# Kernel optimization log

Hardware: AMD Instinct MI355X
Metric: run time of the kernel (lower is better)

## Reference

```python
import jax, jax.numpy as jnp
import numpy as np

ALPHA = 0.2
NEG_INF = -9e15


def setup_inputs() -> dict:
    key = jax.random.key(0)
    k1, k2, k3, k4 = jax.random.split(key, 4)
    B, N, C_IN, C_OUT, R, H = 8, 1024, 256, 256, 4, 4
    node_feats = jax.random.normal(k1, (B, N, C_IN), dtype=jnp.float32)
    adj_matrix = jax.random.randint(k2, (B, N, N, R), 0, 2, dtype=jnp.int32)
    # xavier_uniform with gain=1.414 for Linear(c_in, c_out) weights
    lim_w = 1.414 * np.sqrt(6.0 / (C_IN + C_OUT))
    W = jax.random.uniform(k3, (R, C_IN, C_OUT), minval=-lim_w, maxval=lim_w, dtype=jnp.float32)
    c_per = C_OUT // H
    lim_a = 1.414 * np.sqrt(6.0 / (H + 2 * c_per))
    a = jax.random.uniform(k4, (R, H, 2 * c_per), minval=-lim_a, maxval=lim_a, dtype=jnp.float32)
    return {"node_feats": node_feats, "adj_matrix": adj_matrix, "W": W, "a": a}


def reference(node_feats, adj_matrix, W, a):
    B, N, _ = node_feats.shape
    R, H = a.shape[0], a.shape[1]
    C = a.shape[2] // 2  # per-head feature dim
    out = jnp.zeros((B, N, H, C), dtype=node_feats.dtype)
    for r in range(R):
        # per-relation projection: [B,N,H,C]
        f = jnp.einsum('bnc,cd->bnd', node_feats, W[r]).reshape(B, N, H, C)
        a_l, a_r = a[r, :, :C], a[r, :, C:]
        # attention logit decomposes: a . [f_i || f_j] = a_l . f_i + a_r . f_j
        li = jnp.einsum('bnhc,hc->bnh', f, a_l)  # source-node term
        lj = jnp.einsum('bnhc,hc->bnh', f, a_r)  # target-node term
        logits = jax.nn.leaky_relu(li[:, :, None, :] + lj[:, None, :, :], ALPHA)  # [B,N,N,H]
        mask = adj_matrix[..., r] != 0  # [B,N,N]
        logits = jnp.where(mask[..., None], logits, NEG_INF)
        probs = jax.nn.softmax(logits, axis=2)
        out = out + jnp.einsum('bijh,bjhc->bihc', probs, f)
    # concat_heads=True
    return out.reshape(B, N, H * C)
```

## Files before the change

### kernel.cpp

```cpp
#include <hip/hip_runtime.h>
#include <math.h>

#define Bsz 8
#define Nn 1024
#define CIN 256
#define COUT 256
#define NR 4
#define NH 4

typedef unsigned short u16;
typedef __attribute__((ext_vector_type(8))) short bf16x8;
typedef __attribute__((ext_vector_type(4))) float f32x4;
typedef __attribute__((ext_vector_type(2))) float f32x2;

#define OFF_LIP (16u << 20)
#define OFF_LJP ((16u << 20) + (512u << 10))
#define OFF_ADJM (17u << 20)
#define OFF_XBF (21u << 20)
#define OFF_WBFT (25u << 20)
#define OFF_WAL ((25u << 20) + (512u << 10))
#define OFF_WAR ((25u << 20) + (528u << 10))
#define OFF_OUTR (26u << 20)

#define LOG2E 1.4426950408889634f

__device__ __forceinline__ short f2bf(float x) {
  union { float f; unsigned u; } v; v.f = x;
  unsigned r = (v.u + 0x7FFFu + ((v.u >> 16) & 1u)) >> 16;
  return (short)r;
}

__device__ __forceinline__ float fast_exp2(float x) {
#if __has_builtin(__builtin_amdgcn_exp2f)
  return __builtin_amdgcn_exp2f(x);
#else
  return exp2f(x);
#endif
}

__device__ __forceinline__ int sbfe1(unsigned v, int bit) {
#if __has_builtin(__builtin_amdgcn_sbfe)
  return __builtin_amdgcn_sbfe((int)v, bit, 1);
#else
  return ((int)(v << (31 - bit))) >> 31;
#endif
}

__device__ __forceinline__ unsigned perm_hi16(unsigned hi, unsigned lo) {
#if __has_builtin(__builtin_amdgcn_perm)
  return __builtin_amdgcn_perm(hi, lo, 0x07060302u);
#else
  return (lo >> 16) | (hi & 0xFFFF0000u);
#endif
}

__device__ __forceinline__ void gl_lds16(const void* g, void* l) {
  __builtin_amdgcn_global_load_lds(
      (const __attribute__((address_space(1))) unsigned int*)(unsigned long long)g,
      (__attribute__((address_space(3))) unsigned int*)(unsigned int)(unsigned long long)l,
      16, 0, 0);
}

__global__ __launch_bounds__(256, 8)
void gatt_pack(const int4* __restrict__ adj4, unsigned long long* __restrict__ adjm) {
  const int t = threadIdx.x;
  const int wid = blockIdx.x * 4 + (t >> 6);
  const int lane = t & 63;
  const int jw = wid & 15;
  const int i = (wid >> 4) & 1023;
  const int b = wid >> 14;
  const int j = jw * 64 + lane;
  const int4 av = adj4[(size_t)(b * Nn + i) * Nn + j];
  const unsigned long long b0 = __ballot(av.x != 0);
  const unsigned long long b1 = __ballot(av.y != 0);
  const unsigned long long b2 = __ballot(av.z != 0);
  const unsigned long long b3 = __ballot(av.w != 0);
  if (lane < 4) {
    unsigned long long v = (lane == 0) ? b0 : (lane == 1) ? b1 : (lane == 2) ? b2 : b3;
    adjm[((size_t)((b * Nn + i) * NR + lane)) * 16 + jw] = v;
  }
}

__global__ __launch_bounds__(256, 4)
void gatt_prep(const float* __restrict__ W, const float* __restrict__ a,
               u16* __restrict__ WbfT, float* __restrict__ wa_l,
               float* __restrict__ wa_r) {
  const int t = threadIdx.x;
  if (blockIdx.x < 32) {
    const int r = blockIdx.x >> 3, kc = blockIdx.x & 7;
    u16 pk[32];
#pragma unroll 8
    for (int kk = 0; kk < 32; ++kk)
      pk[kk] = (u16)f2bf(W[(size_t)r * 65536 + (size_t)(kc * 32 + kk) * COUT + t]);
    u16* dst = WbfT + (size_t)r * 65536 + (size_t)t * CIN + kc * 32;
#pragma unroll
    for (int q = 0; q < 4; ++q) *(int4*)(dst + q * 8) = *(int4*)(pk + q * 8);
  } else {
    const int cb = blockIdx.x - 32;
    const int r = cb >> 2, h = cb & 3;
    float sl = 0.f, sr = 0.f;
    const float* Wp = W + (size_t)r * 65536 + (size_t)t * COUT + h * 64;
    const float* ap = a + r * 512 + h * 128;
#pragma unroll 8
    for (int c = 0; c < 64; ++c) {
      const float wv = Wp[c];
      sl = fmaf(wv, ap[c], sl);
      sr = fmaf(wv, ap[64 + c], sr);
    }
    wa_l[(size_t)cb * CIN + t] = sl;
    wa_r[(size_t)cb * CIN + t] = sr;
  }
}

__global__ __launch_bounds__(256, 4)
void gatt_logitx(const float* __restrict__ X, const float4* __restrict__ wal4,
                 const float4* __restrict__ war4, float* __restrict__ Lip,
                 float* __restrict__ Ljp, u16* __restrict__ Xbf) {
  __shared__ float Xs[16 * 260];
  const int t = threadIdx.x;
  const int row0 = blockIdx.x * 16;
  {
    const int il = t >> 4, kq = t & 15;
    const float4* xp = (const float4*)(X + (size_t)(row0 + il) * CIN + kq * 16);
    float4 v[4];
    u16 pk[16];
#pragma unroll
    for (int u = 0; u < 4; ++u) {
      v[u] = xp[u];
      pk[u * 4 + 0] = (u16)f2bf(v[u].x);
      pk[u * 4 + 1] = (u16)f2bf(v[u].y);
      pk[u * 4 + 2] = (u16)f2bf(v[u].z);
      pk[u * 4 + 3] = (u16)f2bf(v[u].w);
    }
    float4* dst = (float4*)(Xs + il * 260 + kq * 16);
#pragma unroll
    for (int u = 0; u < 4; ++u) dst[u] = v[u];
    u16* xb = Xbf + (size_t)(row0 + il) * CIN + kq * 16;
    *(int4*)xb = *(int4*)pk;
    *(int4*)(xb + 8) = *(int4*)(pk + 8);
  }
  __syncthreads();
  const int rl = t >> 4, combo = t & 15;
  float li = 0.f, lj = 0.f;
#pragma unroll 8
  for (int k4 = 0; k4 < 64; ++k4) {
    const float4 x4 = *(const float4*)(Xs + rl * 260 + k4 * 4);
    const float4 wl = wal4[combo * 64 + k4];
    const float4 wr = war4[combo * 64 + k4];
    li += x4.x * wl.x + x4.y * wl.y + x4.z * wl.z + x4.w * wl.w;
    lj += x4.x * wr.x + x4.y * wr.y + x4.z * wr.z + x4.w * wr.w;
  }
  const int g = row0 + rl, b = g >> 10, n = g & 1023;
  const size_t idx = ((size_t)(combo * Bsz + b)) * Nn + n;
  Lip[idx] = li * LOG2E;
  Ljp[idx] = lj * LOG2E;
}

__global__ __launch_bounds__(256)
void gatt_fgemm(const u16* __restrict__ Xbf, const u16* __restrict__ WbfT,
                u16* __restrict__ fTf) {
  __shared__ u16 lds_w[8192];
  __shared__ u16 lds_x[2048];
  const int t = threadIdx.x;
  const int r = blockIdx.x & 3, b = (blockIdx.x >> 2) & 7, ntl = blockIdx.x >> 5;
  const int n0 = ntl * 64;
  const int g0 = b * Nn + n0;
  const int lane = t & 63, w = t >> 6;
  const int m = lane & 15, quad = lane >> 4;
  const int cw = w * 64;
  const int xq = quad ^ (m & 3);

  const u16* Wsrc = WbfT + (size_t)r * 65536;
  f32x4 acc[4][4];
#pragma unroll
  for (int ct = 0; ct < 4; ++ct)
#pragma unroll
    for (int nt = 0; nt < 4; ++nt) acc[ct][nt] = (f32x4){0.f, 0.f, 0.f, 0.f};

  for (int kc = 0; kc < 8; ++kc) {
    __syncthreads();
#pragma unroll
    for (int q = 0; q < 4; ++q) {
      const int s = q * 256 + t;
      const int c = s >> 2, ks = (s & 3) ^ (c & 3);
      gl_lds16(Wsrc + (size_t)c * CIN + kc * 32 + ks * 8, lds_w + s * 8);
    }
    {
      const int s = t;
      const int n = s >> 2, ks = (s & 3) ^ (n & 3);
      gl_lds16(Xbf + (size_t)(g0 + n) * CIN + kc * 32 + ks * 8, lds_x + s * 8);
    }
    __syncthreads();

    bf16x8 af[4], bfr[4];
#pragma unroll
    for (int ct = 0; ct < 4; ++ct)
      af[ct] = *(const bf16x8*)(lds_w + (cw + ct * 16 + m) * 32 + xq * 8);
#pragma unroll
    for (int nt = 0; nt < 4; ++nt)
      bfr[nt] = *(const bf16x8*)(lds_x + (nt * 16 + m) * 32 + xq * 8);
#pragma unroll
    for (int ct = 0; ct < 4; ++ct)
#pragma unroll
      for (int nt = 0; nt < 4; ++nt)
        acc[ct][nt] = __builtin_amdgcn_mfma_f32_16x16x32_bf16(af[ct], bfr[nt], acc[ct][nt], 0, 0, 0);
  }

  u16* fragbase = fTf + (size_t)(((r * Bsz + b) * 4 + w) * 128) * 512;
#pragma unroll
  for (int ct = 0; ct < 4; ++ct) {
#pragma unroll
    for (int ntf = 0; ntf < 4; ++ntf) {
      const int j = n0 + ntf * 16 + m;
      const int jb = j >> 5;
      const int qt = ((ntf & 1) << 1) | (m >> 3);
      const int e = m & 7;
      u16* dst = fragbase + (size_t)((jb * 4 + ct) * 512) + (qt * 16 + quad * 4) * 8 + e;
#pragma unroll
      for (int p = 0; p < 4; ++p) dst[p * 8] = (u16)f2bf(acc[ct][ntf][p]);
    }
  }
}

__global__ __launch_bounds__(256, 4)
void gatt_attn(const unsigned long long* __restrict__ adjm,
               const u16* __restrict__ fTf, const float* __restrict__ Lip,
               const float* __restrict__ Ljp, float* __restrict__ outr) {
  __shared__ float ljs[4 * 1024];

  const int t = threadIdx.x;
  const int comb = blockIdx.x & 31;
  const int b = comb >> 2, r = comb & 3;
  const int i0 = (blockIdx.x >> 5) * 32;
  const int h = t >> 6, lane = t & 63;
  const int m = lane & 15, quad = lane >> 4;
  const int qo = quad * 8;

  {
#pragma unroll
    for (int q = 0; q < 4; ++q) {
      const int s = q * 256 + t;
      const int hh = s >> 8, off = s & 255;
      ((float4*)ljs)[hh * 256 + off] =
          ((const float4*)(Ljp + ((size_t)((r * NH + hh) * Bsz + b)) * Nn))[off];
    }
  }
  __syncthreads();

  const float* lipb = Lip + ((size_t)((r * NH + h) * Bsz + b)) * Nn;
  const float li0 = lipb[i0 + m];
  const float li1 = lipb[i0 + 16 + m];
  const unsigned long long* amp0 = adjm + ((size_t)((b * Nn + i0 + m) * NR + r)) * 16;
  const unsigned long long* amp1 = adjm + ((size_t)((b * Nn + i0 + 16 + m) * NR + r)) * 16;
  const bf16x8* fp = (const bf16x8*)fTf + (size_t)(((r * Bsz + b) * 4 + h)) * 8192;
  const float* ljh = ljs + h * Nn;

  bf16x8 ones;
#pragma unroll
  for (int e = 0; e < 8; ++e) ones[e] = (short)0x3F80;

  f32x4 acc[2][4], den[2];
#pragma unroll
  for (int iw = 0; iw < 2; ++iw) {
    den[iw] = (f32x4){0.f, 0.f, 0.f, 0.f};
#pragma unroll
    for (int nt = 0; nt < 4; ++nt) acc[iw][nt] = (f32x4){0.f, 0.f, 0.f, 0.f};
  }

  for (int jq = 0; jq < 16; ++jq) {
    const uint2 mw0 = *(const uint2*)(amp0 + jq);
    const uint2 mw1 = *(const uint2*)(amp1 + jq);
#pragma unroll
    for (int half = 0; half < 2; ++half) {
      const int jb = jq * 2 + half;
      const unsigned w0 = half ? mw0.y : mw0.x;
      const unsigned w1 = half ? mw1.y : mw1.x;
      const f32x2* lj2p = (const f32x2*)(ljh + jb * 32 + qo);
      bf16x8 bfr[4];
#pragma unroll
      for (int nt = 0; nt < 4; ++nt) bfr[nt] = fp[(jb * 4 + nt) * 64 + lane];
#pragma unroll
      for (int iw = 0; iw < 2; ++iw) {
        const float liv = iw ? li1 : li0;
        const unsigned mb = (iw ? w1 : w0) >> qo;
        const f32x2 li2 = {liv, liv};
        unsigned afu[4];
#pragma unroll
        for (int pr = 0; pr < 4; ++pr) {
          const f32x2 s2 = li2 + lj2p[pr];
          const f32x2 s02 = s2 * 0.2f;
          const float t0 = fmaxf(s2.x, s02.x);
          const float t1 = fmaxf(s2.y, s02.y);
          const unsigned e0 =
              __float_as_uint(fast_exp2(t0)) & (unsigned)sbfe1(mb, 2 * pr);
          const unsigned e1 =
              __float_as_uint(fast_exp2(t1)) & (unsigned)sbfe1(mb, 2 * pr + 1);
          afu[pr] = perm_hi16(e1, e0);
        }
        union { unsigned u[4]; bf16x8 v; } af;
        af.u[0] = afu[0]; af.u[1] = afu[1]; af.u[2] = afu[2]; af.u[3] = afu[3];
        den[iw] = __builtin_amdgcn_mfma_f32_16x16x32_bf16(af.v, ones, den[iw], 0, 0, 0);
#pragma unroll
        for (int nt = 0; nt < 4; ++nt)
          acc[iw][nt] = __builtin_amdgcn_mfma_f32_16x16x32_bf16(af.v, bfr[nt], acc[iw][nt], 0, 0, 0);
      }
    }
  }

#pragma unroll
  for (int iw = 0; iw < 2; ++iw) {
#pragma unroll
    for (int p = 0; p < 4; ++p) {
      const float inv = __builtin_amdgcn_rcpf(den[iw][p]);
      const int i = i0 + iw * 16 + quad * 4 + p;
      float* op = outr + (((size_t)(r * Bsz + b) * Nn) + i) * COUT + h * 64 + m;
#pragma unroll
      for (int nt = 0; nt < 4; ++nt) op[nt * 16] = acc[iw][nt][p] * inv;
    }
  }
}

__global__ __launch_bounds__(256, 8)
void gatt_reduce(const float4* __restrict__ outr4, float4* __restrict__ out4) {
  const int idx = blockIdx.x * 256 + threadIdx.x;
  float4 v0 = outr4[idx];
  float4 v1 = outr4[idx + 524288];
  float4 v2 = outr4[idx + 2 * 524288];
  float4 v3 = outr4[idx + 3 * 524288];
  out4[idx] = make_float4(v0.x + v1.x + v2.x + v3.x, v0.y + v1.y + v2.y + v3.y,
                          v0.z + v1.z + v2.z + v3.z, v0.w + v1.w + v2.w + v3.w);
}

extern "C" void kernel_launch(void* const* d_in, const int* in_sizes, int n_in,
                              void* d_out, int out_size, void* d_ws, size_t ws_size,
                              hipStream_t stream) {
  const float* X = (const float*)d_in[0];
  const int4* adj4 = (const int4*)d_in[1];
  const float* W = (const float*)d_in[2];
  const float* a = (const float*)d_in[3];
  float* out = (float*)d_out;

  char* ws = (char*)d_ws;
  u16* fTf = (u16*)ws;
  float* Lip = (float*)(ws + OFF_LIP);
  float* Ljp = (float*)(ws + OFF_LJP);
  unsigned long long* adjm = (unsigned long long*)(ws + OFF_ADJM);
  u16* Xbf = (u16*)(ws + OFF_XBF);
  u16* WbfT = (u16*)(ws + OFF_WBFT);
  float* wa_l = (float*)(ws + OFF_WAL);
  float* wa_r = (float*)(ws + OFF_WAR);
  float* outr = (float*)(ws + OFF_OUTR);

  gatt_pack<<<dim3(32768), dim3(256), 0, stream>>>(adj4, adjm);
  gatt_prep<<<dim3(48), dim3(256), 0, stream>>>(W, a, WbfT, wa_l, wa_r);
  gatt_logitx<<<dim3(512), dim3(256), 0, stream>>>(X, (const float4*)wa_l,
                                                   (const float4*)wa_r, Lip, Ljp, Xbf);
  gatt_fgemm<<<dim3(512), dim3(256), 0, stream>>>(Xbf, WbfT, fTf);
  gatt_attn<<<dim3(1024), dim3(256), 0, stream>>>(adjm, fTf, Lip, Ljp, outr);
  gatt_reduce<<<dim3(2048), dim3(256), 0, stream>>>((const float4*)outr, (float4*)out);
}
```

Measured before the change: 294.7 us.

## Fuse relation loop into attention, drop reduce kernel, merge pack/prep, LDS-free fgemm

The attention kernel now loops over all four relations per block and accumulates the normalized outputs in registers. This removes the per-relation partial-output buffer and the separate reduction kernel. The pack and weight-prep kernels are merged into one launch. W is pre-laid out in MFMA fragment order so the projection GEMM loads operands directly from global memory without LDS staging. Each attention block now covers 16 rows instead of 32 and no longer caches Lj in LDS, so it issues fewer blocks with less per-block reuse of f fragments.

```diff
diff --git a/kernel.cpp b/kernel.cpp
--- a/kernel.cpp
+++ b/kernel.cpp
@@ -17,10 +17,9 @@
 #define OFF_LJP ((16u << 20) + (512u << 10))
 #define OFF_ADJM (17u << 20)
 #define OFF_XBF (21u << 20)
-#define OFF_WBFT (25u << 20)
+#define OFF_WFRAG (25u << 20)
 #define OFF_WAL ((25u << 20) + (512u << 10))
 #define OFF_WAR ((25u << 20) + (528u << 10))
-#define OFF_OUTR (26u << 20)
 
 #define LOG2E 1.4426950408889634f
 
@@ -54,49 +53,46 @@
 #endif
 }
 
-__device__ __forceinline__ void gl_lds16(const void* g, void* l) {
-  __builtin_amdgcn_global_load_lds(
-      (const __attribute__((address_space(1))) unsigned int*)(unsigned long long)g,
-      (__attribute__((address_space(3))) unsigned int*)(unsigned int)(unsigned long long)l,
-      16, 0, 0);
-}
-
-__global__ __launch_bounds__(256, 8)
-void gatt_pack(const int4* __restrict__ adj4, unsigned long long* __restrict__ adjm) {
+__global__ __launch_bounds__(256, 4)
+void gatt_packprep(const int4* __restrict__ adj4, const float* __restrict__ W,
+                   const float* __restrict__ a, unsigned long long* __restrict__ adjm,
+                   u16* __restrict__ Wfrag, float* __restrict__ wa_l,
+                   float* __restrict__ wa_r) {
   const int t = threadIdx.x;
-  const int wid = blockIdx.x * 4 + (t >> 6);
-  const int lane = t & 63;
-  const int jw = wid & 15;
-  const int i = (wid >> 4) & 1023;
-  const int b = wid >> 14;
-  const int j = jw * 64 + lane;
-  const int4 av = adj4[(size_t)(b * Nn + i) * Nn + j];
-  const unsigned long long b0 = __ballot(av.x != 0);
-  const unsigned long long b1 = __ballot(av.y != 0);
-  const unsigned long long b2 = __ballot(av.z != 0);
-  const unsigned long long b3 = __ballot(av.w != 0);
-  if (lane < 4) {
-    unsigned long long v = (lane == 0) ? b0 : (lane == 1) ? b1 : (lane == 2) ? b2 : b3;
-    adjm[((size_t)((b * Nn + i) * NR + lane)) * 16 + jw] = v;
-  }
-}
-
-__global__ __launch_bounds__(256, 4)
-void gatt_prep(const float* __restrict__ W, const float* __restrict__ a,
-               u16* __restrict__ WbfT, float* __restrict__ wa_l,
-               float* __restrict__ wa_r) {
-  const int t = threadIdx.x;
-  if (blockIdx.x < 32) {
-    const int r = blockIdx.x >> 3, kc = blockIdx.x & 7;
-    u16 pk[32];
+  if (blockIdx.x < 32768) {
+    const int wid = blockIdx.x * 4 + (t >> 6);
+    const int lane = t & 63;
+    const int jw = wid & 15;
+    const int i = (wid >> 4) & 1023;
+    const int b = wid >> 14;
+    const int j = jw * 64 + lane;
+    const int4 av = adj4[(size_t)(b * Nn + i) * Nn + j];
+    const unsigned long long b0 = __ballot(av.x != 0);
+    const unsigned long long b1 = __ballot(av.y != 0);
+    const unsigned long long b2 = __ballot(av.z != 0);
+    const unsigned long long b3 = __ballot(av.w != 0);
+    if (lane < 4) {
+      unsigned long long v = (lane == 0) ? b0 : (lane == 1) ? b1 : (lane == 2) ? b2 : b3;
+      adjm[((size_t)((b * Nn + i) * NR + lane)) * 16 + jw] = v;
+    }
+  } else if (blockIdx.x < 32768 + 32) {
+    const int bid2 = blockIdx.x - 32768;
+    const int r = bid2 >> 3, kc = bid2 & 7;
+    const int cg = t >> 4, mm = t & 15;
+    float wv[32];
 #pragma unroll 8
     for (int kk = 0; kk < 32; ++kk)
-      pk[kk] = (u16)f2bf(W[(size_t)r * 65536 + (size_t)(kc * 32 + kk) * COUT + t]);
-    u16* dst = WbfT + (size_t)r * 65536 + (size_t)t * CIN + kc * 32;
-#pragma unroll
-    for (int q = 0; q < 4; ++q) *(int4*)(dst + q * 8) = *(int4*)(pk + q * 8);
+      wv[kk] = W[(size_t)r * 65536 + (size_t)(kc * 32 + kk) * COUT + t];
+    u16* base = Wfrag + (size_t)r * 65536 + (size_t)(cg * 8 + kc) * 512 + mm * 8;
+#pragma unroll
+    for (int quad = 0; quad < 4; ++quad) {
+      u16 pk[8];
+#pragma unroll
+      for (int e = 0; e < 8; ++e) pk[e] = (u16)f2bf(wv[quad * 8 + e]);
+      *(int4*)(base + quad * 128) = *(int4*)pk;
+    }
   } else {
-    const int cb = blockIdx.x - 32;
+    const int cb = blockIdx.x - 32768 - 32;
     const int r = cb >> 2, h = cb & 3;
     float sl = 0.f, sr = 0.f;
     const float* Wp = W + (size_t)r * 65536 + (size_t)t * COUT + h * 64;
@@ -156,68 +152,51 @@
   Ljp[idx] = lj * LOG2E;
 }
 
-__global__ __launch_bounds__(256)
-void gatt_fgemm(const u16* __restrict__ Xbf, const u16* __restrict__ WbfT,
+__global__ __launch_bounds__(256, 4)
+void gatt_fgemm(const u16* __restrict__ Xbf, const u16* __restrict__ Wfrag,
                 u16* __restrict__ fTf) {
-  __shared__ u16 lds_w[8192];
-  __shared__ u16 lds_x[2048];
   const int t = threadIdx.x;
   const int r = blockIdx.x & 3, b = (blockIdx.x >> 2) & 7, ntl = blockIdx.x >> 5;
-  const int n0 = ntl * 64;
-  const int g0 = b * Nn + n0;
+  const int n0 = ntl * 32;
   const int lane = t & 63, w = t >> 6;
   const int m = lane & 15, quad = lane >> 4;
-  const int cw = w * 64;
-  const int xq = quad ^ (m & 3);
-
-  const u16* Wsrc = WbfT + (size_t)r * 65536;
-  f32x4 acc[4][4];
+
+  const u16* wbase = Wfrag + (size_t)r * 65536 + (size_t)(w * 4) * 8 * 512 + lane * 8;
+  const u16* xbase = Xbf + (size_t)(b * Nn + n0 + m) * CIN + quad * 8;
+
+  f32x4 acc[4][2];
 #pragma unroll
   for (int ct = 0; ct < 4; ++ct)
 #pragma unroll
-    for (int nt = 0; nt < 4; ++nt) acc[ct][nt] = (f32x4){0.f, 0.f, 0.f, 0.f};
-
+    for (int nt = 0; nt < 2; ++nt) acc[ct][nt] = (f32x4){0.f, 0.f, 0.f, 0.f};
+
+#pragma unroll
   for (int kc = 0; kc < 8; ++kc) {
-    __syncthreads();
-#pragma unroll
-    for (int q = 0; q < 4; ++q) {
-      const int s = q * 256 + t;
-      const int c = s >> 2, ks = (s & 3) ^ (c & 3);
-      gl_lds16(Wsrc + (size_t)c * CIN + kc * 32 + ks * 8, lds_w + s * 8);
-    }
-    {
-      const int s = t;
-      const int n = s >> 2, ks = (s & 3) ^ (n & 3);
-      gl_lds16(Xbf + (size_t)(g0 + n) * CIN + kc * 32 + ks * 8, lds_x + s * 8);
-    }
-    __syncthreads();
-
-    bf16x8 af[4], bfr[4];
+    bf16x8 af[4], bfr[2];
 #pragma unroll
     for (int ct = 0; ct < 4; ++ct)
-      af[ct] = *(const bf16x8*)(lds_w + (cw + ct * 16 + m) * 32 + xq * 8);
-#pragma unroll
-    for (int nt = 0; nt < 4; ++nt)
-      bfr[nt] = *(const bf16x8*)(lds_x + (nt * 16 + m) * 32 + xq * 8);
+      af[ct] = *(const bf16x8*)(wbase + (size_t)(ct * 8 + kc) * 512);
+#pragma unroll
+    for (int nt = 0; nt < 2; ++nt)
+      bfr[nt] = *(const bf16x8*)(xbase + (size_t)(nt * 16) * CIN + kc * 32);
 #pragma unroll
     for (int ct = 0; ct < 4; ++ct)
 #pragma unroll
-      for (int nt = 0; nt < 4; ++nt)
+      for (int nt = 0; nt < 2; ++nt)
         acc[ct][nt] = __builtin_amdgcn_mfma_f32_16x16x32_bf16(af[ct], bfr[nt], acc[ct][nt], 0, 0, 0);
   }
 
   u16* fragbase = fTf + (size_t)(((r * Bsz + b) * 4 + w) * 128) * 512;
+  const int jb = n0 >> 5;
+  const int e = m & 7;
 #pragma unroll
   for (int ct = 0; ct < 4; ++ct) {
 #pragma unroll
-    for (int ntf = 0; ntf < 4; ++ntf) {
-      const int j = n0 + ntf * 16 + m;
-      const int jb = j >> 5;
-      const int qt = ((ntf & 1) << 1) | (m >> 3);
-      const int e = m & 7;
+    for (int nt = 0; nt < 2; ++nt) {
+      const int qt = nt * 2 + (m >> 3);
       u16* dst = fragbase + (size_t)((jb * 4 + ct) * 512) + (qt * 16 + quad * 4) * 8 + e;
 #pragma unroll
-      for (int p = 0; p < 4; ++p) dst[p * 8] = (u16)f2bf(acc[ct][ntf][p]);
+      for (int p = 0; p < 4; ++p) dst[p * 8] = (u16)f2bf(acc[ct][nt][p]);
     }
   }
 }
@@ -225,64 +204,45 @@
 __global__ __launch_bounds__(256, 4)
 void gatt_attn(const unsigned long long* __restrict__ adjm,
                const u16* __restrict__ fTf, const float* __restrict__ Lip,
-               const float* __restrict__ Ljp, float* __restrict__ outr) {
-  __shared__ float ljs[4 * 1024];
-
+               const float* __restrict__ Ljp, float* __restrict__ out) {
   const int t = threadIdx.x;
-  const int comb = blockIdx.x & 31;
-  const int b = comb >> 2, r = comb & 3;
-  const int i0 = (blockIdx.x >> 5) * 32;
+  const int b = blockIdx.x & 7;
+  const int i0 = (blockIdx.x >> 3) * 16;
   const int h = t >> 6, lane = t & 63;
   const int m = lane & 15, quad = lane >> 4;
   const int qo = quad * 8;
 
-  {
-#pragma unroll
-    for (int q = 0; q < 4; ++q) {
-      const int s = q * 256 + t;
-      const int hh = s >> 8, off = s & 255;
-      ((float4*)ljs)[hh * 256 + off] =
-          ((const float4*)(Ljp + ((size_t)((r * NH + hh) * Bsz + b)) * Nn))[off];
-    }
-  }
-  __syncthreads();
-
-  const float* lipb = Lip + ((size_t)((r * NH + h) * Bsz + b)) * Nn;
-  const float li0 = lipb[i0 + m];
-  const float li1 = lipb[i0 + 16 + m];
-  const unsigned long long* amp0 = adjm + ((size_t)((b * Nn + i0 + m) * NR + r)) * 16;
-  const unsigned long long* amp1 = adjm + ((size_t)((b * Nn + i0 + 16 + m) * NR + r)) * 16;
-  const bf16x8* fp = (const bf16x8*)fTf + (size_t)(((r * Bsz + b) * 4 + h)) * 8192;
-  const float* ljh = ljs + h * Nn;
-
   bf16x8 ones;
 #pragma unroll
   for (int e = 0; e < 8; ++e) ones[e] = (short)0x3F80;
 
-  f32x4 acc[2][4], den[2];
-#pragma unroll
-  for (int iw = 0; iw < 2; ++iw) {
-    den[iw] = (f32x4){0.f, 0.f, 0.f, 0.f};
-#pragma unroll
-    for (int nt = 0; nt < 4; ++nt) acc[iw][nt] = (f32x4){0.f, 0.f, 0.f, 0.f};
-  }
-
-  for (int jq = 0; jq < 16; ++jq) {
-    const uint2 mw0 = *(const uint2*)(amp0 + jq);
-    const uint2 mw1 = *(const uint2*)(amp1 + jq);
-#pragma unroll
-    for (int half = 0; half < 2; ++half) {
-      const int jb = jq * 2 + half;
-      const unsigned w0 = half ? mw0.y : mw0.x;
-      const unsigned w1 = half ? mw1.y : mw1.x;
-      const f32x2* lj2p = (const f32x2*)(ljh + jb * 32 + qo);
-      bf16x8 bfr[4];
-#pragma unroll
-      for (int nt = 0; nt < 4; ++nt) bfr[nt] = fp[(jb * 4 + nt) * 64 + lane];
-#pragma unroll
-      for (int iw = 0; iw < 2; ++iw) {
-        const float liv = iw ? li1 : li0;
-        const unsigned mb = (iw ? w1 : w0) >> qo;
+  float outsum[4][4];
+#pragma unroll
+  for (int nt = 0; nt < 4; ++nt)
+#pragma unroll
+    for (int p = 0; p < 4; ++p) outsum[nt][p] = 0.f;
+
+  for (int r = 0; r < NR; ++r) {
+    const float liv = Lip[((size_t)((r * NH + h) * Bsz + b)) * Nn + i0 + m];
+    const float* ljh = Ljp + ((size_t)((r * NH + h) * Bsz + b)) * Nn;
+    const unsigned long long* amp = adjm + ((size_t)((b * Nn + i0 + m) * NR + r)) * 16;
+    const bf16x8* fp = (const bf16x8*)fTf + (size_t)((r * Bsz + b) * 4 + h) * 8192;
+
+    f32x4 acc[4], den;
+    den = (f32x4){0.f, 0.f, 0.f, 0.f};
+#pragma unroll
+    for (int nt = 0; nt < 4; ++nt) acc[nt] = (f32x4){0.f, 0.f, 0.f, 0.f};
+
+    for (int jq = 0; jq < 16; ++jq) {
+      const uint2 mw = *(const uint2*)(amp + jq);
+#pragma unroll
+      for (int half = 0; half < 2; ++half) {
+        const int jb = jq * 2 + half;
+        const unsigned mb = (half ? mw.y : mw.x) >> qo;
+        const f32x2* lj2p = (const f32x2*)(ljh + jb * 32 + qo);
+        bf16x8 bfr[4];
+#pragma unroll
+        for (int nt = 0; nt < 4; ++nt) bfr[nt] = fp[(jb * 4 + nt) * 64 + lane];
         const f32x2 li2 = {liv, liv};
         unsigned afu[4];
 #pragma unroll
@@ -299,36 +259,28 @@
         }
         union { unsigned u[4]; bf16x8 v; } af;
         af.u[0] = afu[0]; af.u[1] = afu[1]; af.u[2] = afu[2]; af.u[3] = afu[3];
-        den[iw] = __builtin_amdgcn_mfma_f32_16x16x32_bf16(af.v, ones, den[iw], 0, 0, 0);
+        den = __builtin_amdgcn_mfma_f32_16x16x32_bf16(af.v, ones, den, 0, 0, 0);
 #pragma unroll
         for (int nt = 0; nt < 4; ++nt)
-          acc[iw][nt] = __builtin_amdgcn_mfma_f32_16x16x32_bf16(af.v, bfr[nt], acc[iw][nt], 0, 0, 0);
+          acc[nt] = __builtin_amdgcn_mfma_f32_16x16x32_bf16(af.v, bfr[nt], acc[nt], 0, 0, 0);
       }
     }
-  }
-
-#pragma unroll
-  for (int iw = 0; iw < 2; ++iw) {
+
 #pragma unroll
     for (int p = 0; p < 4; ++p) {
-      const float inv = __builtin_amdgcn_rcpf(den[iw][p]);
-      const int i = i0 + iw * 16 + quad * 4 + p;
-      float* op = outr + (((size_t)(r * Bsz + b) * Nn) + i) * COUT + h * 64 + m;
-#pragma unroll
-      for (int nt = 0; nt < 4; ++nt) op[nt * 16] = acc[iw][nt][p] * inv;
-    }
-  }
-}
-
-__global__ __launch_bounds__(256, 8)
-void gatt_reduce(const float4* __restrict__ outr4, float4* __restrict__ out4) {
-  const int idx = blockIdx.x * 256 + threadIdx.x;
-  float4 v0 = outr4[idx];
-  float4 v1 = outr4[idx + 524288];
-  float4 v2 = outr4[idx + 2 * 524288];
-  float4 v3 = outr4[idx + 3 * 524288];
-  out4[idx] = make_float4(v0.x + v1.x + v2.x + v3.x, v0.y + v1.y + v2.y + v3.y,
-                          v0.z + v1.z + v2.z + v3.z, v0.w + v1.w + v2.w + v3.w);
+      const float inv = __builtin_amdgcn_rcpf(den[p]);
+#pragma unroll
+      for (int nt = 0; nt < 4; ++nt) outsum[nt][p] = fmaf(acc[nt][p], inv, outsum[nt][p]);
+    }
+  }
+
+#pragma unroll
+  for (int p = 0; p < 4; ++p) {
+    const int i = i0 + quad * 4 + p;
+    float* op = out + ((size_t)(b * Nn) + i) * COUT + h * 64 + m;
+#pragma unroll
+    for (int nt = 0; nt < 4; ++nt) op[nt * 16] = outsum[nt][p];
+  }
 }
 
 extern "C" void kernel_launch(void* const* d_in, const int* in_sizes, int n_in,
@@ -346,16 +298,14 @@
   float* Ljp = (float*)(ws + OFF_LJP);
   unsigned long long* adjm = (unsigned long long*)(ws + OFF_ADJM);
   u16* Xbf = (u16*)(ws + OFF_XBF);
-  u16* WbfT = (u16*)(ws + OFF_WBFT);
+  u16* Wfrag = (u16*)(ws + OFF_WFRAG);
   float* wa_l = (float*)(ws + OFF_WAL);
   float* wa_r = (float*)(ws + OFF_WAR);
-  float* outr = (float*)(ws + OFF_OUTR);
-
-  gatt_pack<<<dim3(32768), dim3(256), 0, stream>>>(adj4, adjm);
-  gatt_prep<<<dim3(48), dim3(256), 0, stream>>>(W, a, WbfT, wa_l, wa_r);
+
+  gatt_packprep<<<dim3(32816), dim3(256), 0, stream>>>(adj4, W, a, adjm, Wfrag,
+                                                       wa_l, wa_r);
   gatt_logitx<<<dim3(512), dim3(256), 0, stream>>>(X, (const float4*)wa_l,
                                                    (const float4*)wa_r, Lip, Ljp, Xbf);
-  gatt_fgemm<<<dim3(512), dim3(256), 0, stream>>>(Xbf, WbfT, fTf);
-  gatt_attn<<<dim3(1024), dim3(256), 0, stream>>>(adjm, fTf, Lip, Ljp, outr);
-  gatt_reduce<<<dim3(2048), dim3(256), 0, stream>>>((const float4*)outr, (float4*)out);
-}
+  gatt_fgemm<<<dim3(1024), dim3(256), 0, stream>>>(Xbf, Wfrag, fTf);
+  gatt_attn<<<dim3(512), dim3(256), 0, stream>>>(adjm, fTf, Lip, Ljp, out);
+}
```

Result: slower. 322.0 us (+9.3%).
